# Optimization experiments

Measured on AMD Instinct MI355X. Metric: run time of the kernel, lower is better.

Reference implementation:

```python
import jax, jax.numpy as jnp
import numpy as np

B, S, D, H, HD, FFN_MULT = 4, 2048, 2048, 16, 128, 4
EPS = 1e-8


def setup_inputs() -> dict:
    key = jax.random.key(0)
    ks = jax.random.split(key, 12)
    s = lambda k, shape, scale: (jax.random.normal(k, shape, dtype=jnp.float32) * scale)
    d_ff = D * FFN_MULT
    return {
        "x": s(ks[0], (B, S, D), 1.0),
        # per-head Q/K/V projections, stacked: [H, D, HD] (no bias, as in source)
        "wq": s(ks[1], (H, D, HD), D ** -0.5),
        "wk": s(ks[2], (H, D, HD), D ** -0.5),
        "wv": s(ks[3], (H, D, HD), D ** -0.5),
        # output projection Linear(D, D) with bias
        "wo": s(ks[4], (D, D), D ** -0.5),
        "bo": jnp.zeros((D,), jnp.float32),
        # FFN: Linear(D, d_ff) -> ReLU -> Linear(d_ff, D), both with bias
        "w1": s(ks[5], (D, d_ff), D ** -0.5),
        "b1": jnp.zeros((d_ff,), jnp.float32),
        "w2": s(ks[6], (d_ff, D), d_ff ** -0.5),
        "b2": jnp.zeros((D,), jnp.float32),
        # RMSNorm gains
        "g1": jnp.ones((D,), jnp.float32),
        "g2": jnp.ones((D,), jnp.float32),
    }


def rms_norm(x, g):
    return x * jax.lax.rsqrt(jnp.mean(x * x, axis=-1, keepdims=True) + EPS) * g


def attention(h, wq, wk, wv, wo, bo):
    # per-head projections batched over heads: [B,S,D] x [H,D,K] -> [B,H,S,K]
    q = jnp.einsum("bsd,hdk->bhsk", h, wq)
    k = jnp.einsum("bsd,hdk->bhsk", h, wk)
    v = jnp.einsum("bsd,hdk->bhsk", h, wv)
    scores = jnp.einsum("bhsk,bhtk->bhst", q, k) * (HD ** -0.5)
    causal = jnp.tril(jnp.ones((S, S), dtype=bool))
    scores = jnp.where(causal, scores, -jnp.inf)
    attn = jax.nn.softmax(scores, axis=-1)
    out = jnp.einsum("bhst,bhtk->bhsk", attn, v)  # [B,H,S,HD]
    # concat heads along feature dim (head order matches torch.cat over heads)
    out = out.transpose(0, 2, 1, 3).reshape(B, S, D)
    return out @ wo + bo


def reference(x, wq, wk, wv, wo, bo, w1, b1, w2, b2, g1, g2):
    x = x + attention(rms_norm(x, g1), wq, wk, wv, wo, bo)
    h = rms_norm(x, g2)
    ffn = jax.nn.relu(h @ w1 + b1) @ w2 + b2
    return x + ffn
```

## Files before the change

kernel.cpp:

```cpp
#include <hip/hip_runtime.h>
#include <hip/hip_bf16.h>

#define Bsz 4
#define Ssz 2048
#define Dsz 2048
#define Hn 16
#define HDsz 128
#define DFF 8192
#define Msz (Bsz*Ssz)

typedef __bf16 bf16x8 __attribute__((ext_vector_type(8)));
typedef float  f32x4  __attribute__((ext_vector_type(4)));

enum { FLAG_BIAS=1, FLAG_RELU=2, FLAG_RESID=4, FLAG_F32OUT=8, FLAG_QKV=16 };

#define GLDS16(g, l) __builtin_amdgcn_global_load_lds( \
    (const __attribute__((address_space(1))) unsigned int*)(g), \
    (__attribute__((address_space(3))) unsigned int*)(l), 16, 0, 0)

template <typename TIN>
__global__ __launch_bounds__(256) void transpose_cvt(
    const TIN* __restrict__ in, __bf16* __restrict__ out,
    int R, int C, long long inRS, int subB,
    long long strideOuter, long long strideInner, long long outBS)
{
  __shared__ float tile[32][33];
  int bz = blockIdx.z;
  const TIN* inp = in + (size_t)(bz / subB) * strideOuter + (size_t)(bz % subB) * strideInner;
  __bf16* outp = out + (size_t)bz * outBS;
  int tx = threadIdx.x, ty = threadIdx.y;
  int c  = blockIdx.x * 32 + tx;
  int r0 = blockIdx.y * 32;
#pragma unroll
  for (int i = 0; i < 4; ++i) {
    int r = r0 + ty + i * 8;
    tile[ty + i * 8][tx] = (float)inp[(size_t)r * inRS + c];
  }
  __syncthreads();
  int oc  = r0 + tx;
  int or0 = blockIdx.x * 32;
#pragma unroll
  for (int i = 0; i < 4; ++i) {
    int orr = or0 + ty + i * 8;
    outp[(size_t)orr * R + oc] = (__bf16)tile[tx][ty + i * 8];
  }
}

__global__ __launch_bounds__(256) void rmsnorm_k(
    const float* __restrict__ x, const float* __restrict__ g, __bf16* __restrict__ out)
{
  int row = blockIdx.x, tid = threadIdx.x;
  const float4* xr = (const float4*)(x + (size_t)row * Dsz);
  float4 v0 = xr[tid*2], v1 = xr[tid*2+1];
  float ss = v0.x*v0.x + v0.y*v0.y + v0.z*v0.z + v0.w*v0.w
           + v1.x*v1.x + v1.y*v1.y + v1.z*v1.z + v1.w*v1.w;
#pragma unroll
  for (int off = 32; off > 0; off >>= 1) ss += __shfl_down(ss, off);
  __shared__ float wsum[4];
  __shared__ float sc;
  if ((tid & 63) == 0) wsum[tid >> 6] = ss;
  __syncthreads();
  if (tid == 0) {
    float t = wsum[0] + wsum[1] + wsum[2] + wsum[3];
    sc = rsqrtf(t * (1.0f / (float)Dsz) + 1e-8f);
  }
  __syncthreads();
  float s = sc;
  const float4* gr = (const float4*)g;
  float4 g0 = gr[tid*2], g1v = gr[tid*2+1];
  bf16x8 ov;
  ov[0]=(__bf16)(v0.x*s*g0.x);  ov[1]=(__bf16)(v0.y*s*g0.y);
  ov[2]=(__bf16)(v0.z*s*g0.z);  ov[3]=(__bf16)(v0.w*s*g0.w);
  ov[4]=(__bf16)(v1.x*s*g1v.x); ov[5]=(__bf16)(v1.y*s*g1v.y);
  ov[6]=(__bf16)(v1.z*s*g1v.z); ov[7]=(__bf16)(v1.w*s*g1v.w);
  *(bf16x8*)(out + (size_t)row * Dsz + tid * 8) = ov;
}

#define SBAR       asm volatile("s_barrier" ::: "memory")
#define WAIT_VM3   asm volatile("s_waitcnt vmcnt(3)" ::: "memory")
#define WAIT_VM0   asm volatile("s_waitcnt vmcnt(0)" ::: "memory")

#define STGA(buf, kst) do { \
    GLDS16(Ab + (size_t)(rloc      ) * K + (kst) + sloc, AsB + (buf)*16384 +        wuni); \
    GLDS16(Ab + (size_t)(rloc + 128) * K + (kst) + sloc, AsB + (buf)*16384 + 8192 + wuni); \
  } while (0)
#define STGB(buf, kst) \
    GLDS16(Bb + (size_t)rloc * K + (kst) + sloc, BsB + (buf)*8192 + wuni)

#define LDA(mi) (*(const bf16x8*)(AsB + cur*16384 + (wr*64 + (mi)*16 + l15)*64 + psl))
#define LDB(nj) (*(const bf16x8*)(BsB + cur*8192  + (wc*64 + (nj)*16 + l15)*64 + psl))

__global__ __launch_bounds__(512, 4) void gemm256(
    const __bf16* __restrict__ A, const __bf16* __restrict__ B,
    const float* __restrict__ bias, const float* __restrict__ resid,
    void* __restrict__ Cout, void* __restrict__ CoutV,
    int M, int N, int K, int flags)
{
  __shared__ __align__(16) __bf16 As[3*256*32];
  __shared__ __align__(16) __bf16 Bs[3*128*32];
  int nwg = gridDim.x;
  int id = blockIdx.x;
  id = (id & 7) * (nwg >> 3) + (id >> 3);
  int ntn = N >> 7;
  int tm = id / ntn, tn = id - tm * ntn;
  int tid = threadIdx.x;
  int lane = tid & 63, w = tid >> 6;
  int l15 = lane & 15, lg = lane >> 4;
  int wr = w >> 1, wc = w & 1;
  const __bf16* Ab = A + (size_t)tm * 256 * K;
  const __bf16* Bb = B + (size_t)tn * 128 * K;
  char* AsB = (char*)As;
  char* BsB = (char*)Bs;
  int rloc = tid >> 2;
  int sloc = ((lane & 3) ^ ((lane >> 3) & 3)) * 8;
  int wuni = w * 1024;
  int psl  = (lg ^ ((l15 >> 1) & 3)) * 16;
  f32x4 zero; zero[0]=0.f; zero[1]=0.f; zero[2]=0.f; zero[3]=0.f;
  f32x4 acc[4][4];
#pragma unroll
  for (int i = 0; i < 4; ++i)
#pragma unroll
    for (int j = 0; j < 4; ++j) acc[i][j] = zero;
  int NT = K >> 5;
  STGA(0, 0);  STGB(0, 0);
  STGA(1, 32); STGB(1, 32);
  WAIT_VM3; SBAR;
  int cur = 0;
  for (int t = 0; t < NT; ++t) {
    int sb = cur + 2; if (sb >= 3) sb -= 3;
    int kst = (t + 2 < NT) ? ((t + 2) << 5) : 0;
    STGA(sb, kst);
    STGB(sb, kst);
    bf16x8 af[4], bf[4];
    af[0]=LDA(0); af[1]=LDA(1); af[2]=LDA(2); af[3]=LDA(3);
    bf[0]=LDB(0); bf[1]=LDB(1); bf[2]=LDB(2); bf[3]=LDB(3);
#pragma unroll
    for (int mi = 0; mi < 4; ++mi)
#pragma unroll
      for (int nj = 0; nj < 4; ++nj)
        acc[mi][nj] = __builtin_amdgcn_mfma_f32_16x16x32_bf16(af[mi], bf[nj], acc[mi][nj], 0, 0, 0);
    WAIT_VM3;
    SBAR;
    cur += 1; if (cur >= 3) cur -= 3;
  }
  WAIT_VM0;
  int cm = tm * 256 + wr * 64;
  int cn = tn * 128 + wc * 64;
  float*  Cf = (float*)Cout;
  __bf16* Cb;
  int Ns = N, cnb = cn;
  if (flags & FLAG_QKV) {
    int which = cn >> 11;
    Cb = (which == 2) ? (__bf16*)CoutV
                      : ((__bf16*)Cout + (size_t)which * Msz * 2048);
    Ns = 2048; cnb = cn & 2047;
  } else {
    Cb = (__bf16*)Cout;
  }
#pragma unroll
  for (int m = 0; m < 4; ++m) {
#pragma unroll
    for (int nj = 0; nj < 4; ++nj) {
      int col  = cn  + nj * 16 + l15;
      int colo = cnb + nj * 16 + l15;
      float bv = (flags & FLAG_BIAS) ? bias[col] : 0.0f;
#pragma unroll
      for (int r = 0; r < 4; ++r) {
        int row = cm + m * 16 + 4 * lg + r;
        float v = acc[m][nj][r] + bv;
        if (flags & FLAG_RELU) v = v > 0.f ? v : 0.f;
        size_t idx = (size_t)row * Ns + colo;
        if (flags & FLAG_RESID) v += resid[idx];
        if (flags & FLAG_F32OUT) Cf[idx] = v;
        else                     Cb[idx] = (__bf16)v;
      }
    }
  }
}

__global__ __launch_bounds__(512) void fattn(
    const __bf16* __restrict__ q, const __bf16* __restrict__ k,
    const __bf16* __restrict__ vt, __bf16* __restrict__ o)
{
  __shared__ __align__(16) __bf16 Ks[64*128];
  __shared__ __align__(16) __bf16 Vs[128*64];
  __shared__ __align__(16) __bf16 Ps[8][16*72];
  int bx = blockIdx.x, bh = blockIdx.y;
  int b = bh >> 4, h = bh & 15;
  int tid = threadIdx.x, lane = tid & 63, w = tid >> 6;
  int l15 = lane & 15, lg = lane >> 4;
  size_t base = ((size_t)b * Ssz) * Dsz + (size_t)h * HDsz;
  size_t vtb  = (size_t)bh * HDsz * Ssz;
  const float scale = 0.08838834764831845f;
  char* KsB = (char*)Ks;
  char* VsB = (char*)Vs;
  f32x4 zero; zero[0]=0.f; zero[1]=0.f; zero[2]=0.f; zero[3]=0.f;

  for (int ph = 0; ph < 2; ++ph) {
    int qt = ph ? bx : (15 - bx);
    int qs = qt * 128;
    int qmin = qs + w * 16;
    bf16x8 qf[4];
    int qrow = qmin + l15;
#pragma unroll
    for (int kk = 0; kk < 4; ++kk)
      qf[kk] = *(const bf16x8*)(q + base + (size_t)qrow * Dsz + kk * 32 + lg * 8);
    f32x4 acc[8];
#pragma unroll
    for (int i = 0; i < 8; ++i) acc[i] = zero;
    float mr[4], lr[4];
#pragma unroll
    for (int r = 0; r < 4; ++r) { mr[r] = -1e30f; lr[r] = 0.f; }
    int NT = 2 * qt + 2;
    for (int kt = 0; kt < NT; ++kt) {
      int t0 = kt * 64;
#pragma unroll
      for (int j = 0; j < 2; ++j) {
        int c = tid + j * 512;
        int tr = c >> 4, hc = c & 15;
        bf16x8 tk = *(const bf16x8*)(k + base + (size_t)(t0 + tr) * Dsz + hc * 8);
        *(bf16x8*)(KsB + ((tr * 256 + hc * 16) ^ ((tr & 7) << 4))) = tk;
        int hd = c >> 3, tc = c & 7;
        bf16x8 tv = *(const bf16x8*)(vt + vtb + (size_t)hd * Ssz + t0 + tc * 8);
        *(bf16x8*)(VsB + ((hd * 128 + tc * 16) ^ ((hd & 7) << 4))) = tv;
      }
      __syncthreads();
      bool act = (t0 <= qmin + 15);
      if (act) {
        f32x4 s[4];
#pragma unroll
        for (int cg = 0; cg < 4; ++cg) s[cg] = zero;
        __builtin_amdgcn_s_setprio(1);
#pragma unroll
        for (int kk = 0; kk < 4; ++kk) {
#pragma unroll
          for (int cg = 0; cg < 4; ++cg) {
            int tl = cg * 16 + l15;
            bf16x8 kf = *(const bf16x8*)(KsB + ((tl * 256 + kk * 64 + lg * 16) ^ ((tl & 7) << 4)));
            s[cg] = __builtin_amdgcn_mfma_f32_16x16x32_bf16(qf[kk], kf, s[cg], 0, 0, 0);
          }
        }
        __builtin_amdgcn_s_setprio(0);
        bool nm = (t0 + 63 > qmin);
        float rm[4];
        bool sk = true;
#pragma unroll
        for (int r = 0; r < 4; ++r) {
          int qr = qmin + 4 * lg + r;
          float m0 = -1e30f;
#pragma unroll
          for (int cg = 0; cg < 4; ++cg) {
            float sv = s[cg][r] * scale;
            if (nm && (t0 + cg * 16 + l15) > qr) sv = -1e30f;
            s[cg][r] = sv;
            m0 = fmaxf(m0, sv);
          }
          m0 = fmaxf(m0, __shfl_xor(m0, 1));
          m0 = fmaxf(m0, __shfl_xor(m0, 2));
          m0 = fmaxf(m0, __shfl_xor(m0, 4));
          m0 = fmaxf(m0, __shfl_xor(m0, 8));
          rm[r] = m0;
          sk = sk && (m0 <= mr[r] + 8.0f);
        }
        if (!__all(sk)) {
          f32x4 av;
#pragma unroll
          for (int r = 0; r < 4; ++r) {
            float mn = fmaxf(mr[r], rm[r]);
            float a = __expf(mr[r] - mn);
            mr[r] = mn;
            lr[r] *= a;
            av[r] = a;
          }
#pragma unroll
          for (int hg = 0; hg < 8; ++hg) acc[hg] *= av;
        }
#pragma unroll
        for (int r = 0; r < 4; ++r) {
          float ps = 0.f;
#pragma unroll
          for (int cg = 0; cg < 4; ++cg) {
            float p = __expf(s[cg][r] - mr[r]);
            Ps[w][(4 * lg + r) * 72 + cg * 16 + l15] = (__bf16)p;
            ps += p;
          }
          ps += __shfl_xor(ps, 1);
          ps += __shfl_xor(ps, 2);
          ps += __shfl_xor(ps, 4);
          ps += __shfl_xor(ps, 8);
          lr[r] += ps;
        }
        __builtin_amdgcn_s_setprio(1);
#pragma unroll
        for (int tt = 0; tt < 2; ++tt) {
          bf16x8 pf = *(const bf16x8*)((char*)&Ps[w][0] + l15 * 144 + tt * 64 + lg * 16);
#pragma unroll
          for (int hg = 0; hg < 8; ++hg) {
            int hd = hg * 16 + l15;
            bf16x8 vf = *(const bf16x8*)(VsB + ((hd * 128 + tt * 64 + lg * 16) ^ ((hd & 7) << 4)));
            acc[hg] = __builtin_amdgcn_mfma_f32_16x16x32_bf16(pf, vf, acc[hg], 0, 0, 0);
          }
        }
        __builtin_amdgcn_s_setprio(0);
      }
      __syncthreads();
    }
    f32x4 inv;
#pragma unroll
    for (int r = 0; r < 4; ++r) inv[r] = 1.0f / lr[r];
#pragma unroll
    for (int hg = 0; hg < 8; ++hg) {
      f32x4 ov = acc[hg] * inv;
#pragma unroll
      for (int r = 0; r < 4; ++r) {
        int qr2 = qmin + 4 * lg + r;
        o[base + (size_t)qr2 * Dsz + hg * 16 + l15] = (__bf16)ov[r];
      }
    }
  }
}

extern "C" void kernel_launch(void* const* d_in, const int* in_sizes, int n_in,
                              void* d_out, int out_size, void* d_ws, size_t ws_size,
                              hipStream_t stream)
{
  (void)in_sizes; (void)n_in; (void)out_size; (void)ws_size;
  const float* x  = (const float*)d_in[0];
  const float* wq = (const float*)d_in[1];
  const float* wk = (const float*)d_in[2];
  const float* wv = (const float*)d_in[3];
  const float* wo = (const float*)d_in[4];
  const float* bo = (const float*)d_in[5];
  const float* w1 = (const float*)d_in[6];
  const float* b1 = (const float*)d_in[7];
  const float* w2 = (const float*)d_in[8];
  const float* b2 = (const float*)d_in[9];
  const float* g1 = (const float*)d_in[10];
  const float* g2 = (const float*)d_in[11];
  float* out = (float*)d_out;
  char* ws = (char*)d_ws;

  const size_t U = (size_t)2048 * 2048 * 2;
  __bf16* wqT = (__bf16*)(ws);
  __bf16* wkT = (__bf16*)(ws + U);
  __bf16* wvT = (__bf16*)(ws + 2*U);
  __bf16* woT = (__bf16*)(ws + 3*U);
  __bf16* w1T = (__bf16*)(ws + 4*U);
  __bf16* w2T = (__bf16*)(ws + 8*U);
  __bf16* h1  = (__bf16*)(ws + 12*U);
  __bf16* vb  = (__bf16*)(ws + 16*U);
  __bf16* vT    = h1;
  __bf16* attno = vb;
  __bf16* fb    = h1;
  __bf16* h2    = (__bf16*)(ws);
  __bf16* qb = (__bf16*)d_out;
  __bf16* kb = qb + (size_t)Msz * Dsz;
  float*  x2 = (float*)d_out;

  dim3 tb(32, 8, 1);
  transpose_cvt<float><<<dim3(4,64,16),  tb, 0, stream>>>(wq, wqT, 2048, 128, 128, 1, (long long)2048*128, 0, (long long)128*2048);
  transpose_cvt<float><<<dim3(4,64,16),  tb, 0, stream>>>(wk, wkT, 2048, 128, 128, 1, (long long)2048*128, 0, (long long)128*2048);
  transpose_cvt<float><<<dim3(4,64,16),  tb, 0, stream>>>(wv, wvT, 2048, 128, 128, 1, (long long)2048*128, 0, (long long)128*2048);
  transpose_cvt<float><<<dim3(64,64,1),  tb, 0, stream>>>(wo, woT, 2048, 2048, 2048, 1, 0, 0, 0);
  transpose_cvt<float><<<dim3(256,64,1), tb, 0, stream>>>(w1, w1T, 2048, 8192, 8192, 1, 0, 0, 0);
  transpose_cvt<float><<<dim3(64,128,2), tb, 0, stream>>>(w2, w2T, 4096, 2048, 2048, 1, (long long)4096*2048, 0, (long long)2048*4096);
  rmsnorm_k<<<8192, 256, 0, stream>>>(x, g1, h1);
  gemm256<<<1536, 512, 0, stream>>>(h1, wqT, nullptr, nullptr, qb, vb, Msz, 6144, 2048, FLAG_QKV);
  transpose_cvt<__bf16><<<dim3(4,64,64), tb, 0, stream>>>(vb, vT, 2048, 128, 2048, 16, (long long)2048*2048, 128, (long long)128*2048);
  fattn<<<dim3(8, 64), 512, 0, stream>>>(qb, kb, vT, attno);
  gemm256<<<512, 512, 0, stream>>>(attno, woT, bo, x, x2, nullptr, Msz, 2048, 2048, FLAG_BIAS | FLAG_RESID | FLAG_F32OUT);
  rmsnorm_k<<<8192, 256, 0, stream>>>(x2, g2, h2);
  for (int c = 0; c < 2; ++c) {
    gemm256<<<1024, 512, 0, stream>>>(h2, w1T + (size_t)c*4096*2048, b1 + c*4096, nullptr,
                                      fb, nullptr, Msz, 4096, 2048, FLAG_BIAS | FLAG_RELU);
    int fl = FLAG_RESID | FLAG_F32OUT | (c == 0 ? FLAG_BIAS : 0);
    gemm256<<<512, 512, 0, stream>>>(fb, w2T + (size_t)c*2048*4096, b2, x2,
                                     out, nullptr, Msz, 2048, 4096, fl);
  }
}
```

Baseline: 1.280 ms.

## Use 256x256-tile 1024-thread GEMM for the fused QKV projection

Measured after the change: 1.275 ms. No clear change (-0.4%).

```diff
diff --git a/kernel.cpp b/kernel.cpp
--- a/kernel.cpp
+++ b/kernel.cpp
@@ -17,6 +17,10 @@
 #define GLDS16(g, l) __builtin_amdgcn_global_load_lds( \
     (const __attribute__((address_space(1))) unsigned int*)(g), \
     (__attribute__((address_space(3))) unsigned int*)(l), 16, 0, 0)
+
+#define SBAR       asm volatile("s_barrier" ::: "memory")
+#define WAIT_VM3   asm volatile("s_waitcnt vmcnt(3)" ::: "memory")
+#define WAIT_VM0   asm volatile("s_waitcnt vmcnt(0)" ::: "memory")
 
 template <typename TIN>
 __global__ __launch_bounds__(256) void transpose_cvt(
@@ -76,21 +80,124 @@
   *(bf16x8*)(out + (size_t)row * Dsz + tid * 8) = ov;
 }
 
-#define SBAR       asm volatile("s_barrier" ::: "memory")
-#define WAIT_VM3   asm volatile("s_waitcnt vmcnt(3)" ::: "memory")
-#define WAIT_VM0   asm volatile("s_waitcnt vmcnt(0)" ::: "memory")
-
-#define STGA(buf, kst) do { \
+#define WSTG(Xb, Xlds, buf, kh, kst) \
+    GLDS16((Xb) + (size_t)wrloc * K + (kst) + (kh)*32 + wsloc, (Xlds) + (buf)*32768 + (kh)*16384 + wwuni)
+#define WLDA(kh, mi) (*(const bf16x8*)(AsB + cur*32768 + (kh)*16384 + (wr*64 + (mi)*16 + l15)*64 + psl))
+#define WLDB(kh, nj) (*(const bf16x8*)(BsB + cur*32768 + (kh)*16384 + (wc*64 + (nj)*16 + l15)*64 + psl))
+
+__global__ __launch_bounds__(1024) void gemm_w(
+    const __bf16* __restrict__ A, const __bf16* __restrict__ B,
+    const float* __restrict__ bias, const float* __restrict__ resid,
+    void* __restrict__ Cout, void* __restrict__ CoutV,
+    int M, int N, int K, int flags)
+{
+  __shared__ __align__(16) __bf16 As[2*2*256*32];
+  __shared__ __align__(16) __bf16 Bs[2*2*256*32];
+  int nwg = gridDim.x;
+  int id = blockIdx.x;
+  id = (id & 7) * (nwg >> 3) + (id >> 3);
+  int ntn = N >> 8;
+  int tm = id / ntn, tn = id - tm * ntn;
+  int tid = threadIdx.x;
+  int lane = tid & 63, w = tid >> 6;
+  int l15 = lane & 15, lg = lane >> 4;
+  int wr = w >> 2, wc = w & 3;
+  const __bf16* Ab = A + (size_t)tm * 256 * K;
+  const __bf16* Bb = B + (size_t)tn * 256 * K;
+  char* AsB = (char*)As;
+  char* BsB = (char*)Bs;
+  int wrloc = tid >> 2;
+  int wsloc = ((lane & 3) ^ ((lane >> 3) & 3)) * 8;
+  int wwuni = w * 1024;
+  int psl  = (lg ^ ((l15 >> 1) & 3)) * 16;
+  f32x4 zero; zero[0]=0.f; zero[1]=0.f; zero[2]=0.f; zero[3]=0.f;
+  f32x4 acc[4][4];
+#pragma unroll
+  for (int i = 0; i < 4; ++i)
+#pragma unroll
+    for (int j = 0; j < 4; ++j) acc[i][j] = zero;
+  int NT = K >> 6;
+  WSTG(Ab, AsB, 0, 0, 0);
+  WSTG(Ab, AsB, 0, 1, 0);
+  WSTG(Bb, BsB, 0, 0, 0);
+  WSTG(Bb, BsB, 0, 1, 0);
+  WAIT_VM0; SBAR;
+  int cur = 0;
+  for (int t = 0; t < NT; ++t) {
+    int nb = cur ^ 1;
+    int kst = (t + 1 < NT) ? ((t + 1) << 6) : 0;
+    WSTG(Ab, AsB, nb, 0, kst);
+    WSTG(Ab, AsB, nb, 1, kst);
+    WSTG(Bb, BsB, nb, 0, kst);
+    WSTG(Bb, BsB, nb, 1, kst);
+    {
+      bf16x8 af[4], bf[4];
+      af[0]=WLDA(0,0); af[1]=WLDA(0,1); af[2]=WLDA(0,2); af[3]=WLDA(0,3);
+      bf[0]=WLDB(0,0); bf[1]=WLDB(0,1); bf[2]=WLDB(0,2); bf[3]=WLDB(0,3);
+#pragma unroll
+      for (int mi = 0; mi < 4; ++mi)
+#pragma unroll
+        for (int nj = 0; nj < 4; ++nj)
+          acc[mi][nj] = __builtin_amdgcn_mfma_f32_16x16x32_bf16(af[mi], bf[nj], acc[mi][nj], 0, 0, 0);
+    }
+    {
+      bf16x8 af[4], bf[4];
+      af[0]=WLDA(1,0); af[1]=WLDA(1,1); af[2]=WLDA(1,2); af[3]=WLDA(1,3);
+      bf[0]=WLDB(1,0); bf[1]=WLDB(1,1); bf[2]=WLDB(1,2); bf[3]=WLDB(1,3);
+#pragma unroll
+      for (int mi = 0; mi < 4; ++mi)
+#pragma unroll
+        for (int nj = 0; nj < 4; ++nj)
+          acc[mi][nj] = __builtin_amdgcn_mfma_f32_16x16x32_bf16(af[mi], bf[nj], acc[mi][nj], 0, 0, 0);
+    }
+    WAIT_VM0;
+    SBAR;
+    cur = nb;
+  }
+  int cm = tm * 256 + wr * 64;
+  int cn = tn * 256 + wc * 64;
+  float*  Cf = (float*)Cout;
+  __bf16* Cb;
+  int Ns = N, cnb = cn;
+  if (flags & FLAG_QKV) {
+    int which = cn >> 11;
+    Cb = (which == 2) ? (__bf16*)CoutV
+                      : ((__bf16*)Cout + (size_t)which * Msz * 2048);
+    Ns = 2048; cnb = cn & 2047;
+  } else {
+    Cb = (__bf16*)Cout;
+  }
+#pragma unroll
+  for (int m = 0; m < 4; ++m) {
+#pragma unroll
+    for (int nj = 0; nj < 4; ++nj) {
+      int col  = cn  + nj * 16 + l15;
+      int colo = cnb + nj * 16 + l15;
+      float bv = (flags & FLAG_BIAS) ? bias[col] : 0.0f;
+#pragma unroll
+      for (int r = 0; r < 4; ++r) {
+        int row = cm + m * 16 + 4 * lg + r;
+        float v = acc[m][nj][r] + bv;
+        if (flags & FLAG_RELU) v = v > 0.f ? v : 0.f;
+        size_t idx = (size_t)row * Ns + colo;
+        if (flags & FLAG_RESID) v += resid[idx];
+        if (flags & FLAG_F32OUT) Cf[idx] = v;
+        else                     Cb[idx] = (__bf16)v;
+      }
+    }
+  }
+}
+
+#define NSTGA(buf, kst) do { \
     GLDS16(Ab + (size_t)(rloc      ) * K + (kst) + sloc, AsB + (buf)*16384 +        wuni); \
     GLDS16(Ab + (size_t)(rloc + 128) * K + (kst) + sloc, AsB + (buf)*16384 + 8192 + wuni); \
   } while (0)
-#define STGB(buf, kst) \
+#define NSTGB(buf, kst) \
     GLDS16(Bb + (size_t)rloc * K + (kst) + sloc, BsB + (buf)*8192 + wuni)
-
-#define LDA(mi) (*(const bf16x8*)(AsB + cur*16384 + (wr*64 + (mi)*16 + l15)*64 + psl))
-#define LDB(nj) (*(const bf16x8*)(BsB + cur*8192  + (wc*64 + (nj)*16 + l15)*64 + psl))
-
-__global__ __launch_bounds__(512, 4) void gemm256(
+#define NLDA(mi) (*(const bf16x8*)(AsB + cur*16384 + (wr*64 + (mi)*16 + l15)*64 + psl))
+#define NLDB(nj) (*(const bf16x8*)(BsB + cur*8192  + (wc*64 + (nj)*16 + l15)*64 + psl))
+
+__global__ __launch_bounds__(512, 4) void gemm_n(
     const __bf16* __restrict__ A, const __bf16* __restrict__ B,
     const float* __restrict__ bias, const float* __restrict__ resid,
     void* __restrict__ Cout, void* __restrict__ CoutV,
@@ -122,18 +229,18 @@
 #pragma unroll
     for (int j = 0; j < 4; ++j) acc[i][j] = zero;
   int NT = K >> 5;
-  STGA(0, 0);  STGB(0, 0);
-  STGA(1, 32); STGB(1, 32);
+  NSTGA(0, 0);  NSTGB(0, 0);
+  NSTGA(1, 32); NSTGB(1, 32);
   WAIT_VM3; SBAR;
   int cur = 0;
   for (int t = 0; t < NT; ++t) {
     int sb = cur + 2; if (sb >= 3) sb -= 3;
     int kst = (t + 2 < NT) ? ((t + 2) << 5) : 0;
-    STGA(sb, kst);
-    STGB(sb, kst);
+    NSTGA(sb, kst);
+    NSTGB(sb, kst);
     bf16x8 af[4], bf[4];
-    af[0]=LDA(0); af[1]=LDA(1); af[2]=LDA(2); af[3]=LDA(3);
-    bf[0]=LDB(0); bf[1]=LDB(1); bf[2]=LDB(2); bf[3]=LDB(3);
+    af[0]=NLDA(0); af[1]=NLDA(1); af[2]=NLDA(2); af[3]=NLDA(3);
+    bf[0]=NLDB(0); bf[1]=NLDB(1); bf[2]=NLDB(2); bf[3]=NLDB(3);
 #pragma unroll
     for (int mi = 0; mi < 4; ++mi)
 #pragma unroll
@@ -365,16 +472,16 @@
   transpose_cvt<float><<<dim3(256,64,1), tb, 0, stream>>>(w1, w1T, 2048, 8192, 8192, 1, 0, 0, 0);
   transpose_cvt<float><<<dim3(64,128,2), tb, 0, stream>>>(w2, w2T, 4096, 2048, 2048, 1, (long long)4096*2048, 0, (long long)2048*4096);
   rmsnorm_k<<<8192, 256, 0, stream>>>(x, g1, h1);
-  gemm256<<<1536, 512, 0, stream>>>(h1, wqT, nullptr, nullptr, qb, vb, Msz, 6144, 2048, FLAG_QKV);
+  gemm_w<<<768, 1024, 0, stream>>>(h1, wqT, nullptr, nullptr, qb, vb, Msz, 6144, 2048, FLAG_QKV);
   transpose_cvt<__bf16><<<dim3(4,64,64), tb, 0, stream>>>(vb, vT, 2048, 128, 2048, 16, (long long)2048*2048, 128, (long long)128*2048);
   fattn<<<dim3(8, 64), 512, 0, stream>>>(qb, kb, vT, attno);
-  gemm256<<<512, 512, 0, stream>>>(attno, woT, bo, x, x2, nullptr, Msz, 2048, 2048, FLAG_BIAS | FLAG_RESID | FLAG_F32OUT);
+  gemm_n<<<512, 512, 0, stream>>>(attno, woT, bo, x, x2, nullptr, Msz, 2048, 2048, FLAG_BIAS | FLAG_RESID | FLAG_F32OUT);
   rmsnorm_k<<<8192, 256, 0, stream>>>(x2, g2, h2);
   for (int c = 0; c < 2; ++c) {
-    gemm256<<<1024, 512, 0, stream>>>(h2, w1T + (size_t)c*4096*2048, b1 + c*4096, nullptr,
-                                      fb, nullptr, Msz, 4096, 2048, FLAG_BIAS | FLAG_RELU);
+    gemm_n<<<1024, 512, 0, stream>>>(h2, w1T + (size_t)c*4096*2048, b1 + c*4096, nullptr,
+                                     fb, nullptr, Msz, 4096, 2048, FLAG_BIAS | FLAG_RELU);
     int fl = FLAG_RESID | FLAG_F32OUT | (c == 0 ? FLAG_BIAS : 0);
-    gemm256<<<512, 512, 0, stream>>>(fb, w2T + (size_t)c*2048*4096, b2, x2,
-                                     out, nullptr, Msz, 2048, 4096, fl);
-  }
-}
+    gemm_n<<<512, 512, 0, stream>>>(fb, w2T + (size_t)c*2048*4096, b2, x2,
+                                    out, nullptr, Msz, 2048, 4096, fl);
+  }
+}
```
